# Performance work log

Measured on AMD Instinct MI355X. Metric: run time of the kernel, lower is better.

Reference implementation:

```python
import jax, jax.numpy as jnp
import numpy as np

D = 32      # input_size
H = 256     # hidden_size
B = 4096    # batch
EPS = 1e-12

def _masks(order="A"):
    # Standard MADE degree-based masks. order 'A' = natural ordering.
    deg_in = np.arange(1, D + 1) if order == "A" else np.arange(D, 0, -1)
    deg_h = (np.arange(H) % (D - 1)) + 1
    m0 = (deg_h[None, :] >= deg_in[:, None]).astype(np.float32)  # [D,H] input->hidden
    m1 = (deg_h[None, :] >= deg_h[:, None]).astype(np.float32)   # [H,H] hidden->hidden
    m2 = (deg_in[None, :] > deg_h[:, None]).astype(np.float32)   # [H,D] hidden->output (strict)
    return jnp.asarray(m0), jnp.asarray(m1), jnp.asarray(m2)

M0, M1, M2 = _masks()

def _made(y, W0, b0, W1, b1, W2, b2):
    # masked MLP: D -> H -> H -> D (num_hiddens=2 hidden layers)
    h = jax.nn.relu(y @ (W0 * M0) + b0)
    h = jax.nn.relu(h @ (W1 * M1) + b1)
    return h @ (W2 * M2) + b2

def setup_inputs() -> dict:
    key = jax.random.key(0)
    ks = jax.random.split(key, 8)
    def w(k, fi, fo):
        return jax.random.normal(k, (fi, fo), jnp.float32) / np.sqrt(fi)
    inp = {"x": jax.random.normal(ks[0], (B, D), jnp.float32)}
    i = 1
    for n in ("mu", "lv"):
        inp[n + "_W0"] = w(ks[i], D, H); inp[n + "_b0"] = jnp.zeros((H,), jnp.float32); i += 1
        inp[n + "_W1"] = w(ks[i], H, H); inp[n + "_b1"] = jnp.zeros((H,), jnp.float32); i += 1
        inp[n + "_W2"] = w(ks[i], H, D); inp[n + "_b2"] = jnp.zeros((D,), jnp.float32); i += 1
    return inp

def reference(x, mu_W0, mu_b0, mu_W1, mu_b1, mu_W2, mu_b2,
              lv_W0, lv_b0, lv_W1, lv_b1, lv_W2, lv_b2):
    # AFMADEBlock.forward: D sequential fixed-point iterations of the
    def step(carry, _):
        y, _ls = carry
        mu = _made(y, mu_W0, mu_b0, mu_W1, mu_b1, mu_W2, mu_b2)
        logstd = _made(y, lv_W0, lv_b0, lv_W1, lv_b1, lv_W2, lv_b2) * 0.5
        y_new = (x - mu) / (jnp.exp(logstd) + EPS)
        return (y_new, logstd), None
    init = (jnp.zeros_like(x), jnp.zeros_like(x))
    (y, logstd), _ = jax.lax.scan(step, init, None, length=D)
    return y, logstd.sum(axis=1)
```

## Files before the change

### kernel.cpp

```cpp
#include <hip/hip_runtime.h>

#define DD   32
#define HH   256
#define BB   4096
#define RR   2
#define EPSF 1e-12f

__device__ __forceinline__ int made_pi(int p) {
    return (p < 72) ? (p / 9) + 31 * (p % 9)
                    : (8 + (p - 72) / 8) + 31 * ((p - 72) % 8);
}
__device__ __forceinline__ int made_off(int d) {
    return (d <= 9) ? 9 * (d - 1) : 8 * d;
}

#define NW0   (DD * HH)
#define NW1   (HH * HH)
#define NETF  (NW0 + NW1 + HH + HH)
#define W2IOFF (2 * NETF)
#define NW2I  (HH * 64)
#define WSNEED ((size_t)(W2IOFF + NW2I) * 4)

__global__ void made_prep(
    const float* __restrict__ muW0, const float* __restrict__ mub0,
    const float* __restrict__ muW1, const float* __restrict__ mub1,
    const float* __restrict__ muW2,
    const float* __restrict__ lvW0, const float* __restrict__ lvb0,
    const float* __restrict__ lvW1, const float* __restrict__ lvb1,
    const float* __restrict__ lvW2,
    float* __restrict__ ws)
{
    const int t = threadIdx.x;
    const int b = blockIdx.x;
    __shared__ float rowbuf[HH];

    if (b < 512) {
        const int n = b >> 8, p = b & 255;
        const int h = made_pi(p);
        const float* W1 = n ? lvW1 : muW1;
        float* o = ws + (size_t)n * NETF;
        *reinterpret_cast<float4*>(&rowbuf[4 * t]) =
            *reinterpret_cast<const float4*>(W1 + h * HH + 4 * t);
        __syncthreads();
        float4 w;
        w.x = rowbuf[made_pi(4 * t + 0)];
        w.y = rowbuf[made_pi(4 * t + 1)];
        w.z = rowbuf[made_pi(4 * t + 2)];
        w.w = rowbuf[made_pi(4 * t + 3)];
        *reinterpret_cast<float4*>(o + NW0 + p * HH + 4 * t) = w;
        if (t == 0) {
            o[NW0 + NW1 + p]      = (n ? lvb0 : mub0)[h];
            o[NW0 + NW1 + HH + p] = (n ? lvb1 : mub1)[h];
        }
    } else if (b < 768) {
        const int p = b - 512;
        const int h = made_pi(p);
        const int n = t >> 5, dd = t & 31;
        ws[W2IOFF + p * 64 + t] = (n ? lvW2 : muW2)[h * DD + dd];
    } else {
        const int idx = b - 768;
        const int n = idx >> 5, i = idx & 31;
        const float* W0 = n ? lvW0 : muW0;
        float* o = ws + (size_t)n * NETF;
        *reinterpret_cast<float4*>(&rowbuf[4 * t]) =
            *reinterpret_cast<const float4*>(W0 + i * HH + 4 * t);
        __syncthreads();
        float4 w;
        w.x = rowbuf[made_pi(4 * t + 0)];
        w.y = rowbuf[made_pi(4 * t + 1)];
        w.z = rowbuf[made_pi(4 * t + 2)];
        w.w = rowbuf[made_pi(4 * t + 3)];
        *reinterpret_cast<float4*>(o + i * HH + 4 * t) = w;
    }
}

__global__ __launch_bounds__(256, 2) void made_main(
    const float* __restrict__ ws, const float* __restrict__ x,
    const float* __restrict__ mub2, const float* __restrict__ lvb2,
    float* __restrict__ out)
{
    const int lane = threadIdx.x & 63;
    const int wv   = threadIdx.x >> 6;
    const int row0 = ((blockIdx.x << 2) + wv) * RR;
    const int c4   = lane << 2;
    const int nn   = lane >> 5;
    const int ddl  = lane & 31;

    const float* W0p[2] = {ws,       ws + NETF};
    const float* W1p[2] = {ws + NW0, ws + NETF + NW0};
    const float* W2i    = ws + W2IOFF;

    float h0[2][4][RR], h1[2][4][RR];
    #pragma unroll
    for (int n = 0; n < 2; ++n) {
        const float* bb = ws + (size_t)n * NETF + NW0 + NW1;
        const float4 v0 = *reinterpret_cast<const float4*>(bb + c4);
        const float4 v1 = *reinterpret_cast<const float4*>(bb + HH + c4);
        const float a0[4] = {v0.x, v0.y, v0.z, v0.w};
        const float a1[4] = {v1.x, v1.y, v1.z, v1.w};
        #pragma unroll
        for (int s = 0; s < 4; ++s)
            #pragma unroll
            for (int r = 0; r < RR; ++r) { h0[n][s][r] = a0[s]; h1[n][s][r] = a1[s]; }
    }

    const float accinit = nn ? lvb2[ddl] : mub2[ddl];
    float acc[RR];
    #pragma unroll
    for (int r = 0; r < RR; ++r) acc[r] = accinit;

    float xvr[RR];
    #pragma unroll
    for (int r = 0; r < RR; ++r) xvr[r] = x[(row0 + r) * DD + ddl];

    __shared__ float A[4][2][RR][12];
    __shared__ float Bf[4][2][RR][12];

    float yprev[RR], lsum[RR], ysave[RR];
    #pragma unroll
    for (int r = 0; r < RR; ++r) { lsum[r] = 0.f; ysave[r] = 0.f; }

    #pragma unroll
    for (int r = 0; r < RR; ++r) {
        const float mu  = __shfl(acc[r], 0, 64);
        const float lv  = __shfl(acc[r], 32, 64);
        const float ls2 = 0.5f * lv;
        lsum[r] += ls2;
        const float yd = (__shfl(xvr[r], 0, 64) - mu) / (__expf(ls2) + EPSF);
        yprev[r] = yd;
        if (lane == 0) ysave[r] = yd;
    }

    for (int d = 1; d < DD; ++d) {
        const int off = made_off(d);
        const int nk  = (d <= 8) ? 9 : 8;
        int r8 = off + 8; if (r8 > 255) r8 = 255;

        const float4 w0m = *reinterpret_cast<const float4*>(W0p[0] + (d - 1) * HH + c4);
        const float4 w0l = *reinterpret_cast<const float4*>(W0p[1] + (d - 1) * HH + c4);
        float4 w1m[9], w1l[9];
        {
            const float* a = W1p[0] + off * HH + c4;
            const float* b = W1p[1] + off * HH + c4;
            #pragma unroll
            for (int k = 0; k < 8; ++k) {
                w1m[k] = *reinterpret_cast<const float4*>(a + k * HH);
                w1l[k] = *reinterpret_cast<const float4*>(b + k * HH);
            }
            w1m[8] = *reinterpret_cast<const float4*>(W1p[0] + r8 * HH + c4);
            w1l[8] = *reinterpret_cast<const float4*>(W1p[1] + r8 * HH + c4);
        }
        float w2[9];
        {
            const float* w2c = W2i + off * 64 + lane;
            #pragma unroll
            for (int k = 0; k < 8; ++k) w2[k] = w2c[k * 64];
            w2[8] = W2i[r8 * 64 + lane];
        }

        #pragma unroll
        for (int r = 0; r < RR; ++r) {
            h0[0][0][r] = fmaf(yprev[r], w0m.x, h0[0][0][r]);
            h0[0][1][r] = fmaf(yprev[r], w0m.y, h0[0][1][r]);
            h0[0][2][r] = fmaf(yprev[r], w0m.z, h0[0][2][r]);
            h0[0][3][r] = fmaf(yprev[r], w0m.w, h0[0][3][r]);
            h0[1][0][r] = fmaf(yprev[r], w0l.x, h0[1][0][r]);
            h0[1][1][r] = fmaf(yprev[r], w0l.y, h0[1][1][r]);
            h0[1][2][r] = fmaf(yprev[r], w0l.z, h0[1][2][r]);
            h0[1][3][r] = fmaf(yprev[r], w0l.w, h0[1][3][r]);
        }

        if (d >= 9 && lane == 0) {
            #pragma unroll
            for (int n = 0; n < 2; ++n)
                #pragma unroll
                for (int r = 0; r < RR; ++r) {
                    A[wv][n][r][8]  = 0.f;
                    Bf[wv][n][r][8] = 0.f;
                }
        }
        #pragma unroll
        for (int s = 0; s < 4; ++s) {
            const int k = c4 + s - off;
            if ((unsigned)k < (unsigned)nk) {
                #pragma unroll
                for (int r = 0; r < RR; ++r) {
                    A[wv][0][r][k] = fmaxf(h0[0][s][r], 0.f);
                    A[wv][1][r][k] = fmaxf(h0[1][s][r], 0.f);
                }
            }
        }
        float av[2][RR][9];
        #pragma unroll
        for (int n = 0; n < 2; ++n)
            #pragma unroll
            for (int r = 0; r < RR; ++r) {
                const float4 a03 = *reinterpret_cast<const float4*>(&A[wv][n][r][0]);
                const float4 a47 = *reinterpret_cast<const float4*>(&A[wv][n][r][4]);
                av[n][r][0] = a03.x; av[n][r][1] = a03.y;
                av[n][r][2] = a03.z; av[n][r][3] = a03.w;
                av[n][r][4] = a47.x; av[n][r][5] = a47.y;
                av[n][r][6] = a47.z; av[n][r][7] = a47.w;
                av[n][r][8] = A[wv][n][r][8];
            }

        #pragma unroll
        for (int k = 0; k < 9; ++k) {
            #pragma unroll
            for (int r = 0; r < RR; ++r) {
                h1[0][0][r] = fmaf(av[0][r][k], w1m[k].x, h1[0][0][r]);
                h1[0][1][r] = fmaf(av[0][r][k], w1m[k].y, h1[0][1][r]);
                h1[0][2][r] = fmaf(av[0][r][k], w1m[k].z, h1[0][2][r]);
                h1[0][3][r] = fmaf(av[0][r][k], w1m[k].w, h1[0][3][r]);
                h1[1][0][r] = fmaf(av[1][r][k], w1l[k].x, h1[1][0][r]);
                h1[1][1][r] = fmaf(av[1][r][k], w1l[k].y, h1[1][1][r]);
                h1[1][2][r] = fmaf(av[1][r][k], w1l[k].z, h1[1][2][r]);
                h1[1][3][r] = fmaf(av[1][r][k], w1l[k].w, h1[1][3][r]);
            }
        }

        #pragma unroll
        for (int s = 0; s < 4; ++s) {
            const int k = c4 + s - off;
            if ((unsigned)k < (unsigned)nk) {
                #pragma unroll
                for (int r = 0; r < RR; ++r) {
                    Bf[wv][0][r][k] = fmaxf(h1[0][s][r], 0.f);
                    Bf[wv][1][r][k] = fmaxf(h1[1][s][r], 0.f);
                }
            }
        }
        float rb[RR][9];
        #pragma unroll
        for (int r = 0; r < RR; ++r) {
            const float4 b03 = *reinterpret_cast<const float4*>(&Bf[wv][nn][r][0]);
            const float4 b47 = *reinterpret_cast<const float4*>(&Bf[wv][nn][r][4]);
            rb[r][0] = b03.x; rb[r][1] = b03.y; rb[r][2] = b03.z; rb[r][3] = b03.w;
            rb[r][4] = b47.x; rb[r][5] = b47.y; rb[r][6] = b47.z; rb[r][7] = b47.w;
            rb[r][8] = Bf[wv][nn][r][8];
        }
        #pragma unroll
        for (int k = 0; k < 9; ++k)
            #pragma unroll
            for (int r = 0; r < RR; ++r)
                acc[r] = fmaf(rb[r][k], w2[k], acc[r]);

        #pragma unroll
        for (int r = 0; r < RR; ++r) {
            const float mu  = __shfl(acc[r], d, 64);
            const float lv  = __shfl(acc[r], 32 + d, 64);
            const float ls2 = 0.5f * lv;
            lsum[r] += ls2;
            const float yd = (__shfl(xvr[r], d, 64) - mu) / (__expf(ls2) + EPSF);
            yprev[r] = yd;
            if (lane == d) ysave[r] = yd;
        }
    }

    #pragma unroll
    for (int r = 0; r < RR; ++r) {
        if (lane < DD) out[(row0 + r) * DD + lane] = ysave[r];
        if (lane == 0) out[BB * DD + row0 + r] = lsum[r];
    }
}

__global__ __launch_bounds__(64, 1) void made_inv_fb(
    const float* __restrict__ x,
    const float* __restrict__ muW0, const float* __restrict__ mub0,
    const float* __restrict__ muW1, const float* __restrict__ mub1,
    const float* __restrict__ muW2, const float* __restrict__ mub2,
    const float* __restrict__ lvW0, const float* __restrict__ lvb0,
    const float* __restrict__ lvW1, const float* __restrict__ lvb1,
    const float* __restrict__ lvW2, const float* __restrict__ lvb2,
    float* __restrict__ out)
{
    const int lane    = threadIdx.x;
    const int rowBase = blockIdx.x * 4;
    const int hb      = lane << 2;
    int deg[4];
    #pragma unroll
    for (int s = 0; s < 4; ++s) deg[s] = ((hb + s) % 31) + 1;
    const float* Wp0[2] = {muW0, lvW0};
    const float* Bp0[2] = {mub0, lvb0};
    const float* Wp1[2] = {muW1, lvW1};
    const float* Bp1[2] = {mub1, lvb1};
    const float* Wp2[2] = {muW2, lvW2};
    float h0pre[2][4][4], h1pre[2][4][4], r1[2][4][4], yprev[4], lsum[4];
    #pragma unroll
    for (int n = 0; n < 2; ++n) {
        const float4 b0v = *reinterpret_cast<const float4*>(Bp0[n] + hb);
        const float4 b1v = *reinterpret_cast<const float4*>(Bp1[n] + hb);
        const float b0a[4] = {b0v.x, b0v.y, b0v.z, b0v.w};
        const float b1a[4] = {b1v.x, b1v.y, b1v.z, b1v.w};
        #pragma unroll
        for (int s = 0; s < 4; ++s)
            #pragma unroll
            for (int r = 0; r < 4; ++r) {
                h0pre[n][s][r] = b0a[s]; h1pre[n][s][r] = b1a[s]; r1[n][s][r] = 0.f;
            }
    }
    #pragma unroll
    for (int r = 0; r < 4; ++r) { yprev[r] = 0.f; lsum[r] = 0.f; }
    __shared__ float lds_a[2][4][12];
    for (int d = 0; d < DD; ++d) {
        if (d >= 1) {
            #pragma unroll
            for (int n = 0; n < 2; ++n) {
                const float4 w0 = *reinterpret_cast<const float4*>(Wp0[n] + (d - 1) * HH + hb);
                const float w0a[4] = {w0.x, w0.y, w0.z, w0.w};
                #pragma unroll
                for (int s = 0; s < 4; ++s)
                    #pragma unroll
                    for (int r = 0; r < 4; ++r)
                        h0pre[n][s][r] = fmaf(yprev[r], w0a[s], h0pre[n][s][r]);
            }
            #pragma unroll
            for (int n = 0; n < 2; ++n)
                #pragma unroll
                for (int s = 0; s < 4; ++s)
                    if (deg[s] == d) {
                        const int k = (hb + s - (d - 1)) / 31;
                        #pragma unroll
                        for (int r = 0; r < 4; ++r)
                            lds_a[n][r][k] = fmaxf(h0pre[n][s][r], 0.f);
                    }
            __syncthreads();
            const bool nine = (d <= 8);
            #pragma unroll
            for (int n = 0; n < 2; ++n) {
                const float* W1r = Wp1[n] + (size_t)(d - 1) * HH + hb;
                float4 w1v[9];
                #pragma unroll
                for (int k = 0; k < 8; ++k)
                    w1v[k] = *reinterpret_cast<const float4*>(W1r + k * 31 * HH);
                if (nine) w1v[8] = *reinterpret_cast<const float4*>(W1r + 8 * 31 * HH);
                #pragma unroll
                for (int r = 0; r < 4; ++r) {
                    const float4 a03 = *reinterpret_cast<const float4*>(&lds_a[n][r][0]);
                    const float4 a47 = *reinterpret_cast<const float4*>(&lds_a[n][r][4]);
                    const float av[8] = {a03.x, a03.y, a03.z, a03.w, a47.x, a47.y, a47.z, a47.w};
                    #pragma unroll
                    for (int k = 0; k < 8; ++k) {
                        const float wk[4] = {w1v[k].x, w1v[k].y, w1v[k].z, w1v[k].w};
                        #pragma unroll
                        for (int s = 0; s < 4; ++s)
                            h1pre[n][s][r] = fmaf(av[k], wk[s], h1pre[n][s][r]);
                    }
                    if (nine) {
                        const float a8 = lds_a[n][r][8];
                        const float wk[4] = {w1v[8].x, w1v[8].y, w1v[8].z, w1v[8].w};
                        #pragma unroll
                        for (int s = 0; s < 4; ++s)
                            h1pre[n][s][r] = fmaf(a8, wk[s], h1pre[n][s][r]);
                    }
                }
            }
            #pragma unroll
            for (int n = 0; n < 2; ++n)
                #pragma unroll
                for (int s = 0; s < 4; ++s)
                    if (deg[s] == d)
                        #pragma unroll
                        for (int r = 0; r < 4; ++r)
                            r1[n][s][r] = fmaxf(h1pre[n][s][r], 0.f);
            __syncthreads();
        }
        float w2v[2][4];
        #pragma unroll
        for (int n = 0; n < 2; ++n)
            #pragma unroll
            for (int s = 0; s < 4; ++s)
                w2v[n][s] = Wp2[n][(hb + s) * DD + d];
        float red[2][4];
        #pragma unroll
        for (int n = 0; n < 2; ++n)
            #pragma unroll
            for (int r = 0; r < 4; ++r) {
                float p = 0.f;
                #pragma unroll
                for (int s = 0; s < 4; ++s) p = fmaf(r1[n][s][r], w2v[n][s], p);
                red[n][r] = p;
            }
        #pragma unroll
        for (int m = 1; m < 64; m <<= 1)
            #pragma unroll
            for (int n = 0; n < 2; ++n)
                #pragma unroll
                for (int r = 0; r < 4; ++r)
                    red[n][r] += __shfl_xor(red[n][r], m, 64);
        const float b2m = mub2[d], b2l = lvb2[d];
        #pragma unroll
        for (int r = 0; r < 4; ++r) {
            const float mu = red[0][r] + b2m;
            const float logstd = 0.5f * (red[1][r] + b2l);
            lsum[r] += logstd;
            const float yd = (x[(rowBase + r) * DD + d] - mu) / (__expf(logstd) + EPSF);
            yprev[r] = yd;
            if (lane == 0) out[(rowBase + r) * DD + d] = yd;
        }
    }
    if (lane == 0)
        #pragma unroll
        for (int r = 0; r < 4; ++r) out[BB * DD + rowBase + r] = lsum[r];
}

extern "C" void kernel_launch(void* const* d_in, const int* in_sizes, int n_in,
                              void* d_out, int out_size, void* d_ws, size_t ws_size,
                              hipStream_t stream) {
    const float* x    = (const float*)d_in[0];
    const float* muW0 = (const float*)d_in[1];
    const float* mub0 = (const float*)d_in[2];
    const float* muW1 = (const float*)d_in[3];
    const float* mub1 = (const float*)d_in[4];
    const float* muW2 = (const float*)d_in[5];
    const float* mub2 = (const float*)d_in[6];
    const float* lvW0 = (const float*)d_in[7];
    const float* lvb0 = (const float*)d_in[8];
    const float* lvW1 = (const float*)d_in[9];
    const float* lvb1 = (const float*)d_in[10];
    const float* lvW2 = (const float*)d_in[11];
    const float* lvb2 = (const float*)d_in[12];
    float* out = (float*)d_out;

    if (ws_size >= WSNEED) {
        float* ws = (float*)d_ws;
        made_prep<<<dim3(832), dim3(64), 0, stream>>>(
            muW0, mub0, muW1, mub1, muW2,
            lvW0, lvb0, lvW1, lvb1, lvW2, ws);
        made_main<<<dim3(BB / (4 * RR)), dim3(256), 0, stream>>>(ws, x, mub2, lvb2, out);
    } else {
        made_inv_fb<<<dim3(BB / 4), dim3(64), 0, stream>>>(x,
            muW0, mub0, muW1, mub1, muW2, mub2,
            lvW0, lvb0, lvW1, lvb1, lvW2, lvb2, out);
    }
}
```

Before: 135.9 us.

## Stage per-step MADE weights in double-buffered LDS shared across waves

Rather than each wave loading its own copy of the W0/W1/W2 slices from global memory every step, the four waves in a block load the next step's slice cooperatively into a double-buffered shared-memory area, prefetching one step ahead. Each wave then reads its weights from LDS. This cuts redundant global and L2 traffic fourfold and hides load latency behind compute. The cost is about 45 KB of LDS per block, which may limit occupancy under launch_bounds(256,2), plus a block-wide barrier every step.

```diff
diff --git a/kernel.cpp b/kernel.cpp
--- a/kernel.cpp
+++ b/kernel.cpp
@@ -20,6 +20,8 @@
 #define W2IOFF (2 * NETF)
 #define NW2I  (HH * 64)
 #define WSNEED ((size_t)(W2IOFF + NW2I) * 4)
+
+#define BUFSZ 5696
 
 __global__ void made_prep(
     const float* __restrict__ muW0, const float* __restrict__ mub0,
@@ -90,6 +92,10 @@
     const float* W1p[2] = {ws + NW0, ws + NETF + NW0};
     const float* W2i    = ws + W2IOFF;
 
+    __shared__ float sbuf[2 * BUFSZ];
+    __shared__ float A [4][2][RR][12];
+    __shared__ float Bf[4][2][RR][12];
+
     float h0[2][4][RR], h1[2][4][RR];
     #pragma unroll
     for (int n = 0; n < 2; ++n) {
@@ -112,9 +118,6 @@
     float xvr[RR];
     #pragma unroll
     for (int r = 0; r < RR; ++r) xvr[r] = x[(row0 + r) * DD + ddl];
-
-    __shared__ float A[4][2][RR][12];
-    __shared__ float Bf[4][2][RR][12];
 
     float yprev[RR], lsum[RR], ysave[RR];
     #pragma unroll
@@ -131,32 +134,76 @@
         if (lane == 0) ysave[r] = yd;
     }
 
+    {
+        const int offD = 0;
+        #pragma unroll
+        for (int i = 0; i < 6; ++i) {
+            const int c = wv + 4 * i;
+            if (c < 22) {
+                const float* src;
+                if (c < 18) {
+                    const int n = c / 9, k = c - n * 9;
+                    src = W1p[n] + (offD + k) * HH;
+                } else if (c < 20) {
+                    src = W0p[c - 18];
+                } else {
+                    src = W2i + offD * 64 + (c - 20) * 256;
+                }
+                const float4 v = *reinterpret_cast<const float4*>(src + c4);
+                *reinterpret_cast<float4*>(&sbuf[c * 256 + c4]) = v;
+            } else if (c == 22) {
+                sbuf[5632 + lane] = W2i[(offD + 8) * 64 + lane];
+            }
+        }
+    }
+    __syncthreads();
+
+    int cur = 0;
     for (int d = 1; d < DD; ++d) {
         const int off = made_off(d);
         const int nk  = (d <= 8) ? 9 : 8;
-        int r8 = off + 8; if (r8 > 255) r8 = 255;
-
-        const float4 w0m = *reinterpret_cast<const float4*>(W0p[0] + (d - 1) * HH + c4);
-        const float4 w0l = *reinterpret_cast<const float4*>(W0p[1] + (d - 1) * HH + c4);
+
+        float4 pf[6];
+        float  pfs = 0.f;
+        const bool haveNext = (d < DD - 1);
+        if (haveNext) {
+            const int dd2  = d + 1;
+            const int offD = made_off(dd2);
+            #pragma unroll
+            for (int i = 0; i < 6; ++i) {
+                const int c = wv + 4 * i;
+                if (c < 22) {
+                    const float* src;
+                    if (c < 18) {
+                        const int n = c / 9, k = c - n * 9;
+                        int row = offD + k; if (row > 255) row = 255;
+                        src = W1p[n] + row * HH;
+                    } else if (c < 20) {
+                        src = W0p[c - 18] + (dd2 - 1) * HH;
+                    } else {
+                        src = W2i + offD * 64 + (c - 20) * 256;
+                    }
+                    pf[i] = *reinterpret_cast<const float4*>(src + c4);
+                } else if (c == 22) {
+                    int r8 = offD + 8; if (r8 > 255) r8 = 255;
+                    pfs = W2i[r8 * 64 + lane];
+                }
+            }
+        }
+
+        const float* cb = &sbuf[cur * BUFSZ];
+
+        const float4 w0m = *reinterpret_cast<const float4*>(&cb[18 * 256 + c4]);
+        const float4 w0l = *reinterpret_cast<const float4*>(&cb[19 * 256 + c4]);
         float4 w1m[9], w1l[9];
-        {
-            const float* a = W1p[0] + off * HH + c4;
-            const float* b = W1p[1] + off * HH + c4;
-            #pragma unroll
-            for (int k = 0; k < 8; ++k) {
-                w1m[k] = *reinterpret_cast<const float4*>(a + k * HH);
-                w1l[k] = *reinterpret_cast<const float4*>(b + k * HH);
-            }
-            w1m[8] = *reinterpret_cast<const float4*>(W1p[0] + r8 * HH + c4);
-            w1l[8] = *reinterpret_cast<const float4*>(W1p[1] + r8 * HH + c4);
+        #pragma unroll
+        for (int k = 0; k < 9; ++k) {
+            w1m[k] = *reinterpret_cast<const float4*>(&cb[k * 256 + c4]);
+            w1l[k] = *reinterpret_cast<const float4*>(&cb[(9 + k) * 256 + c4]);
         }
         float w2[9];
-        {
-            const float* w2c = W2i + off * 64 + lane;
-            #pragma unroll
-            for (int k = 0; k < 8; ++k) w2[k] = w2c[k * 64];
-            w2[8] = W2i[r8 * 64 + lane];
-        }
+        #pragma unroll
+        for (int k = 0; k < 9; ++k) w2[k] = cb[5120 + k * 64 + lane];
 
         #pragma unroll
         for (int r = 0; r < RR; ++r) {
@@ -255,6 +302,18 @@
             yprev[r] = yd;
             if (lane == d) ysave[r] = yd;
         }
+
+        if (haveNext) {
+            float* nb = &sbuf[(cur ^ 1) * BUFSZ];
+            #pragma unroll
+            for (int i = 0; i < 6; ++i) {
+                const int c = wv + 4 * i;
+                if (c < 22)       *reinterpret_cast<float4*>(&nb[c * 256 + c4]) = pf[i];
+                else if (c == 22) nb[5632 + lane] = pfs;
+            }
+        }
+        __syncthreads();
+        cur ^= 1;
     }
 
     #pragma unroll
```

Result: slower. 199.8 us (+47.0%).

## Double-buffer per-step weight slices into LDS via async global_load_lds prefetch

Applied to the files above, without the earlier changes.

Each step's W0/W1/W2 weight slices are now staged into a double-buffered shared-memory area using global_load_lds, with step d+1 prefetched while step d computes. Blocks share the staged slices instead of every wave issuing its own global loads, which is meant to hide the global latency on the serial critical path. In exchange it adds a block-wide __syncthreads per step and about 45KB of LDS per block. That LDS use may cut the occupancy of 2 blocks per CU, and the per-step barrier adds sync cost.

```diff
diff --git a/kernel.cpp b/kernel.cpp
--- a/kernel.cpp
+++ b/kernel.cpp
@@ -20,6 +20,19 @@
 #define W2IOFF (2 * NETF)
 #define NW2I  (HH * 64)
 #define WSNEED ((size_t)(W2IOFF + NW2I) * 4)
+
+#define BUFSZ 5696
+
+__device__ __forceinline__ void glds16(float* lds, const float* g) {
+    __builtin_amdgcn_global_load_lds(
+        (const __attribute__((address_space(1))) void*)g,
+        (__attribute__((address_space(3))) void*)lds, 16, 0, 0);
+}
+__device__ __forceinline__ void glds4(float* lds, const float* g) {
+    __builtin_amdgcn_global_load_lds(
+        (const __attribute__((address_space(1))) void*)g,
+        (__attribute__((address_space(3))) void*)lds, 4, 0, 0);
+}
 
 __global__ void made_prep(
     const float* __restrict__ muW0, const float* __restrict__ mub0,
@@ -90,6 +103,10 @@
     const float* W1p[2] = {ws + NW0, ws + NETF + NW0};
     const float* W2i    = ws + W2IOFF;
 
+    __shared__ float sbuf[2 * BUFSZ];
+    __shared__ float A [4][2][RR][12];
+    __shared__ float Bf[4][2][RR][12];
+
     float h0[2][4][RR], h1[2][4][RR];
     #pragma unroll
     for (int n = 0; n < 2; ++n) {
@@ -112,9 +129,6 @@
     float xvr[RR];
     #pragma unroll
     for (int r = 0; r < RR; ++r) xvr[r] = x[(row0 + r) * DD + ddl];
-
-    __shared__ float A[4][2][RR][12];
-    __shared__ float Bf[4][2][RR][12];
 
     float yprev[RR], lsum[RR], ysave[RR];
     #pragma unroll
@@ -131,32 +145,44 @@
         if (lane == 0) ysave[r] = yd;
     }
 
+    auto stage_step = [&](float* nb, int dd) {
+        const int offD = made_off(dd);
+        #pragma unroll
+        for (int i = 0; i < 6; ++i) {
+            const int c = wv + 4 * i;
+            if (c < 22) {
+                const float* src;
+                if (c < 18) {
+                    const int n = c / 9, k = c - n * 9;
+                    int row = offD + k; if (row > 255) row = 255;
+                    src = W1p[n] + row * HH;
+                } else if (c < 20) {
+                    src = W0p[c - 18] + (dd - 1) * HH;
+                } else {
+                    src = W2i + offD * 64 + (c - 20) * 256;
+                }
+                glds16(&sbuf[0] + (nb - &sbuf[0]) + c * 256, src + c4);
+            }
+        }
+        if (wv == 2) {
+            int r8 = offD + 8; if (r8 > 255) r8 = 255;
+            glds4(nb + 22 * 256, W2i + r8 * 64 + lane);
+        }
+    };
+
+    stage_step(&sbuf[0], 1);
+    __syncthreads();
+
+    int cur = 0;
     for (int d = 1; d < DD; ++d) {
         const int off = made_off(d);
         const int nk  = (d <= 8) ? 9 : 8;
-        int r8 = off + 8; if (r8 > 255) r8 = 255;
-
-        const float4 w0m = *reinterpret_cast<const float4*>(W0p[0] + (d - 1) * HH + c4);
-        const float4 w0l = *reinterpret_cast<const float4*>(W0p[1] + (d - 1) * HH + c4);
-        float4 w1m[9], w1l[9];
-        {
-            const float* a = W1p[0] + off * HH + c4;
-            const float* b = W1p[1] + off * HH + c4;
-            #pragma unroll
-            for (int k = 0; k < 8; ++k) {
-                w1m[k] = *reinterpret_cast<const float4*>(a + k * HH);
-                w1l[k] = *reinterpret_cast<const float4*>(b + k * HH);
-            }
-            w1m[8] = *reinterpret_cast<const float4*>(W1p[0] + r8 * HH + c4);
-            w1l[8] = *reinterpret_cast<const float4*>(W1p[1] + r8 * HH + c4);
-        }
-        float w2[9];
-        {
-            const float* w2c = W2i + off * 64 + lane;
-            #pragma unroll
-            for (int k = 0; k < 8; ++k) w2[k] = w2c[k * 64];
-            w2[8] = W2i[r8 * 64 + lane];
-        }
+        float* cb = &sbuf[cur * BUFSZ];
+
+        if (d < DD - 1) stage_step(&sbuf[(cur ^ 1) * BUFSZ], d + 1);
+
+        const float4 w0m = *reinterpret_cast<const float4*>(&cb[18 * 256 + c4]);
+        const float4 w0l = *reinterpret_cast<const float4*>(&cb[19 * 256 + c4]);
 
         #pragma unroll
         for (int r = 0; r < RR; ++r) {
@@ -206,16 +232,18 @@
 
         #pragma unroll
         for (int k = 0; k < 9; ++k) {
+            const float4 wm = *reinterpret_cast<const float4*>(&cb[k * 256 + c4]);
+            const float4 wl = *reinterpret_cast<const float4*>(&cb[(9 + k) * 256 + c4]);
             #pragma unroll
             for (int r = 0; r < RR; ++r) {
-                h1[0][0][r] = fmaf(av[0][r][k], w1m[k].x, h1[0][0][r]);
-                h1[0][1][r] = fmaf(av[0][r][k], w1m[k].y, h1[0][1][r]);
-                h1[0][2][r] = fmaf(av[0][r][k], w1m[k].z, h1[0][2][r]);
-                h1[0][3][r] = fmaf(av[0][r][k], w1m[k].w, h1[0][3][r]);
-                h1[1][0][r] = fmaf(av[1][r][k], w1l[k].x, h1[1][0][r]);
-                h1[1][1][r] = fmaf(av[1][r][k], w1l[k].y, h1[1][1][r]);
-                h1[1][2][r] = fmaf(av[1][r][k], w1l[k].z, h1[1][2][r]);
-                h1[1][3][r] = fmaf(av[1][r][k], w1l[k].w, h1[1][3][r]);
+                h1[0][0][r] = fmaf(av[0][r][k], wm.x, h1[0][0][r]);
+                h1[0][1][r] = fmaf(av[0][r][k], wm.y, h1[0][1][r]);
+                h1[0][2][r] = fmaf(av[0][r][k], wm.z, h1[0][2][r]);
+                h1[0][3][r] = fmaf(av[0][r][k], wm.w, h1[0][3][r]);
+                h1[1][0][r] = fmaf(av[1][r][k], wl.x, h1[1][0][r]);
+                h1[1][1][r] = fmaf(av[1][r][k], wl.y, h1[1][1][r]);
+                h1[1][2][r] = fmaf(av[1][r][k], wl.z, h1[1][2][r]);
+                h1[1][3][r] = fmaf(av[1][r][k], wl.w, h1[1][3][r]);
             }
         }
 
@@ -240,10 +268,18 @@
             rb[r][8] = Bf[wv][nn][r][8];
         }
         #pragma unroll
-        for (int k = 0; k < 9; ++k)
+        for (int k = 0; k < 8; ++k) {
+            const float w2k = cb[5120 + k * 64 + lane];
             #pragma unroll
             for (int r = 0; r < RR; ++r)
-                acc[r] = fmaf(rb[r][k], w2[k], acc[r]);
+                acc[r] = fmaf(rb[r][k], w2k, acc[r]);
+        }
+        {
+            const float w2t = cb[5632 + lane];
+            #pragma unroll
+            for (int r = 0; r < RR; ++r)
+                acc[r] = fmaf(rb[r][8], w2t, acc[r]);
+        }
 
         #pragma unroll
         for (int r = 0; r < RR; ++r) {
@@ -255,6 +291,9 @@
             yprev[r] = yd;
             if (lane == d) ysave[r] = yd;
         }
+
+        __syncthreads();
+        cur ^= 1;
     }
 
     #pragma unroll
```

Result: slower. 172.0 us (+26.5%).

## Prefetch next-step weights into registers and use single-wave blocks

Applied to the files above, without the earlier changes.

Weight rows for step d+1 are now loaded into registers while step d computes, so their global load latency overlaps the FMA work. The first step's weights are preloaded before the loop. Blocks shrink from four waves to one wave, with shared scratch per block. The divide by exp(ls)+eps becomes a multiply by exp(-ls). Double-buffering the weights roughly doubles their register footprint, which may lower occupancy or cause spills. Dropping eps changes numerics only slightly.

```diff
diff --git a/kernel.cpp b/kernel.cpp
--- a/kernel.cpp
+++ b/kernel.cpp
@@ -74,14 +74,13 @@
     }
 }
 
-__global__ __launch_bounds__(256, 2) void made_main(
+__global__ __launch_bounds__(64, 2) void made_main(
     const float* __restrict__ ws, const float* __restrict__ x,
     const float* __restrict__ mub2, const float* __restrict__ lvb2,
     float* __restrict__ out)
 {
-    const int lane = threadIdx.x & 63;
-    const int wv   = threadIdx.x >> 6;
-    const int row0 = ((blockIdx.x << 2) + wv) * RR;
+    const int lane = threadIdx.x;
+    const int row0 = blockIdx.x * RR;
     const int c4   = lane << 2;
     const int nn   = lane >> 5;
     const int ddl  = lane & 31;
@@ -89,6 +88,9 @@
     const float* W0p[2] = {ws,       ws + NETF};
     const float* W1p[2] = {ws + NW0, ws + NETF + NW0};
     const float* W2i    = ws + W2IOFF;
+
+    __shared__ float A [2][RR][12];
+    __shared__ float Bf[2][RR][12];
 
     float h0[2][4][RR], h1[2][4][RR];
     #pragma unroll
@@ -113,9 +115,6 @@
     #pragma unroll
     for (int r = 0; r < RR; ++r) xvr[r] = x[(row0 + r) * DD + ddl];
 
-    __shared__ float A[4][2][RR][12];
-    __shared__ float Bf[4][2][RR][12];
-
     float yprev[RR], lsum[RR], ysave[RR];
     #pragma unroll
     for (int r = 0; r < RR; ++r) { lsum[r] = 0.f; ysave[r] = 0.f; }
@@ -126,37 +125,27 @@
         const float lv  = __shfl(acc[r], 32, 64);
         const float ls2 = 0.5f * lv;
         lsum[r] += ls2;
-        const float yd = (__shfl(xvr[r], 0, 64) - mu) / (__expf(ls2) + EPSF);
+        const float yd = (__shfl(xvr[r], 0, 64) - mu) * __expf(-ls2);
         yprev[r] = yd;
         if (lane == 0) ysave[r] = yd;
+    }
+
+    float4 w0m, w0l, w1m[9], w1l[9];
+    float  w2[9];
+    {
+        w0m = *reinterpret_cast<const float4*>(W0p[0] + c4);
+        w0l = *reinterpret_cast<const float4*>(W0p[1] + c4);
+        #pragma unroll
+        for (int k = 0; k < 9; ++k) {
+            w1m[k] = *reinterpret_cast<const float4*>(W1p[0] + k * HH + c4);
+            w1l[k] = *reinterpret_cast<const float4*>(W1p[1] + k * HH + c4);
+            w2[k]  = W2i[k * 64 + lane];
+        }
     }
 
     for (int d = 1; d < DD; ++d) {
         const int off = made_off(d);
         const int nk  = (d <= 8) ? 9 : 8;
-        int r8 = off + 8; if (r8 > 255) r8 = 255;
-
-        const float4 w0m = *reinterpret_cast<const float4*>(W0p[0] + (d - 1) * HH + c4);
-        const float4 w0l = *reinterpret_cast<const float4*>(W0p[1] + (d - 1) * HH + c4);
-        float4 w1m[9], w1l[9];
-        {
-            const float* a = W1p[0] + off * HH + c4;
-            const float* b = W1p[1] + off * HH + c4;
-            #pragma unroll
-            for (int k = 0; k < 8; ++k) {
-                w1m[k] = *reinterpret_cast<const float4*>(a + k * HH);
-                w1l[k] = *reinterpret_cast<const float4*>(b + k * HH);
-            }
-            w1m[8] = *reinterpret_cast<const float4*>(W1p[0] + r8 * HH + c4);
-            w1l[8] = *reinterpret_cast<const float4*>(W1p[1] + r8 * HH + c4);
-        }
-        float w2[9];
-        {
-            const float* w2c = W2i + off * 64 + lane;
-            #pragma unroll
-            for (int k = 0; k < 8; ++k) w2[k] = w2c[k * 64];
-            w2[8] = W2i[r8 * 64 + lane];
-        }
 
         #pragma unroll
         for (int r = 0; r < RR; ++r) {
@@ -175,8 +164,8 @@
             for (int n = 0; n < 2; ++n)
                 #pragma unroll
                 for (int r = 0; r < RR; ++r) {
-                    A[wv][n][r][8]  = 0.f;
-                    Bf[wv][n][r][8] = 0.f;
+                    A[n][r][8]  = 0.f;
+                    Bf[n][r][8] = 0.f;
                 }
         }
         #pragma unroll
@@ -185,8 +174,8 @@
             if ((unsigned)k < (unsigned)nk) {
                 #pragma unroll
                 for (int r = 0; r < RR; ++r) {
-                    A[wv][0][r][k] = fmaxf(h0[0][s][r], 0.f);
-                    A[wv][1][r][k] = fmaxf(h0[1][s][r], 0.f);
+                    A[0][r][k] = fmaxf(h0[0][s][r], 0.f);
+                    A[1][r][k] = fmaxf(h0[1][s][r], 0.f);
                 }
             }
         }
@@ -195,13 +184,13 @@
         for (int n = 0; n < 2; ++n)
             #pragma unroll
             for (int r = 0; r < RR; ++r) {
-                const float4 a03 = *reinterpret_cast<const float4*>(&A[wv][n][r][0]);
-                const float4 a47 = *reinterpret_cast<const float4*>(&A[wv][n][r][4]);
+                const float4 a03 = *reinterpret_cast<const float4*>(&A[n][r][0]);
+                const float4 a47 = *reinterpret_cast<const float4*>(&A[n][r][4]);
                 av[n][r][0] = a03.x; av[n][r][1] = a03.y;
                 av[n][r][2] = a03.z; av[n][r][3] = a03.w;
                 av[n][r][4] = a47.x; av[n][r][5] = a47.y;
                 av[n][r][6] = a47.z; av[n][r][7] = a47.w;
-                av[n][r][8] = A[wv][n][r][8];
+                av[n][r][8] = A[n][r][8];
             }
 
         #pragma unroll
@@ -219,25 +208,42 @@
             }
         }
 
+        const int dn   = (d < DD - 1) ? d + 1 : DD - 1;
+        const int offN = made_off(dn);
+        int r8n = offN + 8; if (r8n > 255) r8n = 255;
+        float4 nw0m = *reinterpret_cast<const float4*>(W0p[0] + (dn - 1) * HH + c4);
+        float4 nw0l = *reinterpret_cast<const float4*>(W0p[1] + (dn - 1) * HH + c4);
+        float4 nw1m[9], nw1l[9];
+        float  nw2[9];
+        #pragma unroll
+        for (int k = 0; k < 8; ++k) {
+            nw1m[k] = *reinterpret_cast<const float4*>(W1p[0] + (offN + k) * HH + c4);
+            nw1l[k] = *reinterpret_cast<const float4*>(W1p[1] + (offN + k) * HH + c4);
+            nw2[k]  = W2i[(offN + k) * 64 + lane];
+        }
+        nw1m[8] = *reinterpret_cast<const float4*>(W1p[0] + r8n * HH + c4);
+        nw1l[8] = *reinterpret_cast<const float4*>(W1p[1] + r8n * HH + c4);
+        nw2[8]  = W2i[r8n * 64 + lane];
+
         #pragma unroll
         for (int s = 0; s < 4; ++s) {
             const int k = c4 + s - off;
             if ((unsigned)k < (unsigned)nk) {
                 #pragma unroll
                 for (int r = 0; r < RR; ++r) {
-                    Bf[wv][0][r][k] = fmaxf(h1[0][s][r], 0.f);
-                    Bf[wv][1][r][k] = fmaxf(h1[1][s][r], 0.f);
+                    Bf[0][r][k] = fmaxf(h1[0][s][r], 0.f);
+                    Bf[1][r][k] = fmaxf(h1[1][s][r], 0.f);
                 }
             }
         }
         float rb[RR][9];
         #pragma unroll
         for (int r = 0; r < RR; ++r) {
-            const float4 b03 = *reinterpret_cast<const float4*>(&Bf[wv][nn][r][0]);
-            const float4 b47 = *reinterpret_cast<const float4*>(&Bf[wv][nn][r][4]);
+            const float4 b03 = *reinterpret_cast<const float4*>(&Bf[nn][r][0]);
+            const float4 b47 = *reinterpret_cast<const float4*>(&Bf[nn][r][4]);
             rb[r][0] = b03.x; rb[r][1] = b03.y; rb[r][2] = b03.z; rb[r][3] = b03.w;
             rb[r][4] = b47.x; rb[r][5] = b47.y; rb[r][6] = b47.z; rb[r][7] = b47.w;
-            rb[r][8] = Bf[wv][nn][r][8];
+            rb[r][8] = Bf[nn][r][8];
         }
         #pragma unroll
         for (int k = 0; k < 9; ++k)
@@ -251,9 +257,15 @@
             const float lv  = __shfl(acc[r], 32 + d, 64);
             const float ls2 = 0.5f * lv;
             lsum[r] += ls2;
-            const float yd = (__shfl(xvr[r], d, 64) - mu) / (__expf(ls2) + EPSF);
+            const float yd = (__shfl(xvr[r], d, 64) - mu) * __expf(-ls2);
             yprev[r] = yd;
             if (lane == d) ysave[r] = yd;
+        }
+
+        w0m = nw0m; w0l = nw0l;
+        #pragma unroll
+        for (int k = 0; k < 9; ++k) {
+            w1m[k] = nw1m[k]; w1l[k] = nw1l[k]; w2[k] = nw2[k];
         }
     }
 
@@ -427,7 +439,7 @@
         made_prep<<<dim3(832), dim3(64), 0, stream>>>(
             muW0, mub0, muW1, mub1, muW2,
             lvW0, lvb0, lvW1, lvb1, lvW2, ws);
-        made_main<<<dim3(BB / (4 * RR)), dim3(256), 0, stream>>>(ws, x, mub2, lvb2, out);
+        made_main<<<dim3(BB / RR), dim3(64), 0, stream>>>(ws, x, mub2, lvb2, out);
     } else {
         made_inv_fb<<<dim3(BB / 4), dim3(64), 0, stream>>>(x,
             muW0, mub0, muW1, mub1, muW2, mub2,
```

Result: slower. 175.1 us (+28.8%).
